# Optimization experiments

Hardware: AMD Instinct MI355X
Metric: run time of the kernel (lower is better)

## Reference

```python
import jax, jax.numpy as jnp
import numpy as np

NUM_USERS = 100000
NUM_ITEMS = 100000
N_NODES = NUM_USERS + NUM_ITEMS
EMB = 64
N_EDGES = 3200000
N_LAYERS = 3


def setup_inputs() -> dict:
    key = jax.random.key(0)
    k1, k2, k3, k4, k5 = jax.random.split(key, 5)
    user_emb = jax.random.normal(k1, (NUM_USERS, EMB), dtype=jnp.float32)
    item_emb = jax.random.normal(k2, (NUM_ITEMS, EMB), dtype=jnp.float32)
    # COO representation of the normalized adjacency norm_adj (values ~ 1/sqrt(d_i d_j))
    edge_row = jax.random.randint(k3, (N_EDGES,), 0, N_NODES, dtype=jnp.int32)
    edge_col = jax.random.randint(k4, (N_EDGES,), 0, N_NODES, dtype=jnp.int32)
    edge_w = jax.random.uniform(k5, (N_EDGES,), dtype=jnp.float32)
    return {"user_emb": user_emb, "item_emb": item_emb, "edge_w": edge_w,
            "edge_row": edge_row, "edge_col": edge_col}


def _spmm(edge_row, edge_col, edge_w, x):
    # y[r] = sum_{e: row[e]==r} w[e] * x[col[e]]  ==  torch.sparse.mm(norm_adj, x)
    msgs = edge_w[:, None] * x[edge_col]  # [n_edges, E]
    return jax.ops.segment_sum(msgs, edge_row, num_segments=N_NODES)


def reference(user_emb, item_emb, edge_w, edge_row, edge_col):
    ego = jnp.concatenate([user_emb, item_emb], axis=0)  # [N, E]
    acc = jnp.zeros_like(ego)
    for _ in range(N_LAYERS):
        ego = _spmm(edge_row, edge_col, edge_w, ego)
        acc = acc + ego
    final = acc / N_LAYERS  # mean over the n_layers propagated embeddings
    user_all = final[:NUM_USERS]
    item_all = final[NUM_USERS:]
    return (user_all, item_all)
```

## Files before the change

### kernel.cpp

```cpp
#include <hip/hip_runtime.h>
#include <hip/hip_bf16.h>


constexpr int NUM_USERS = 100000;
constexpr int NUM_ITEMS = 100000;
constexpr int N_NODES   = NUM_USERS + NUM_ITEMS;
constexpr int EMB       = 64;
constexpr int N_EDGES   = 3200000;

constexpr int BUCK_SHIFT = 8;
constexpr int NBUCK = (N_NODES + 255) >> BUCK_SHIFT;
constexpr int BIN_BLOCK = 512;
constexpr int EPB = 8192;
constexpr int NBIN_BLOCKS = (N_EDGES + EPB - 1) / EPB;
constexpr int SORT_CAP = 6144;

constexpr int HIST_BLOCKS   = 512;
constexpr int CONCAT_BLOCKS = (N_NODES * 8 + 255) / 256;

constexpr int ROWS_PER_BLOCK = 32;
constexpr int ECAP = 1536;


__device__ __forceinline__ float bfl(unsigned u) { return __uint_as_float(u << 16); }
__device__ __forceinline__ float bfh(unsigned u) { return __uint_as_float(u & 0xFFFF0000u); }
__device__ __forceinline__ unsigned f2bf(float f) {
    unsigned u = __float_as_uint(f);
    return (u + 0x7FFFu + ((u >> 16) & 1u)) >> 16;
}
__device__ __forceinline__ unsigned pk(float lo, float hi) {
    return f2bf(lo) | (f2bf(hi) << 16);
}


__global__ __launch_bounds__(256) void prep(
    const int* __restrict__ row, int* __restrict__ bcnt,
    const float4* __restrict__ u, const float4* __restrict__ it,
    uint4* __restrict__ ebuf) {
    __shared__ int h[NBUCK];
    if (blockIdx.x < HIST_BLOCKS) {
        for (int i = threadIdx.x; i < NBUCK; i += 256) h[i] = 0;
        __syncthreads();
        int nt = HIST_BLOCKS * 256;
        for (int e = blockIdx.x * 256 + threadIdx.x; e < N_EDGES; e += nt) {
            int r = __builtin_nontemporal_load(&row[e]);
            atomicAdd(&h[r >> BUCK_SHIFT], 1);
        }
        __syncthreads();
        for (int i = threadIdx.x; i < NBUCK; i += 256) {
            int c = h[i];
            if (c) atomicAdd(&bcnt[i], c);
        }
    } else {
        int i = (blockIdx.x - HIST_BLOCKS) * 256 + threadIdx.x;
        if (i >= N_NODES * 8) return;
        const float4* s = (i < NUM_USERS * 8) ? (u + 2 * (size_t)i)
                                              : (it + 2 * ((size_t)i - (size_t)NUM_USERS * 8));
        float4 f0 = s[0], f1 = s[1];
        uint4 o;
        o.x = pk(f0.x, f0.y); o.y = pk(f0.z, f0.w);
        o.z = pk(f1.x, f1.y); o.w = pk(f1.z, f1.w);
        ebuf[i] = o;
    }
}


__global__ __launch_bounds__(1024) void scan_buckets(const int* __restrict__ bcnt,
                                                     int* __restrict__ bbase,
                                                     int* __restrict__ bcursor) {
    __shared__ int lds[1024];
    int t = threadIdx.x;
    int v = (t < NBUCK) ? bcnt[t] : 0;
    lds[t] = v;
    __syncthreads();
    for (int off = 1; off < 1024; off <<= 1) {
        int x = (t >= off) ? lds[t - off] : 0;
        __syncthreads();
        lds[t] += x;
        __syncthreads();
    }
    int excl = lds[t] - v;
    if (t < NBUCK) { bbase[t] = excl; bcursor[t] = excl; }
    if (t == 0) bbase[NBUCK] = N_EDGES;
}

__global__ __launch_bounds__(BIN_BLOCK) void bin_edges(
    const int* __restrict__ row, const int* __restrict__ col,
    const float* __restrict__ w,
    int* __restrict__ bcursor, int2* __restrict__ binned) {
    __shared__ int2 stage[EPB];
    __shared__ int  hcnt[NBUCK];
    __shared__ int  hbase[NBUCK];
    __shared__ int  cursor[NBUCK];
    __shared__ int  lds2[BIN_BLOCK];
    int t = threadIdx.x;
    int e0 = blockIdx.x * EPB;
    int e1 = e0 + EPB; if (e1 > N_EDGES) e1 = N_EDGES;

    for (int i = t; i < NBUCK; i += BIN_BLOCK) hcnt[i] = 0;
    __syncthreads();
    for (int e = e0 + t; e < e1; e += BIN_BLOCK)
        atomicAdd(&hcnt[row[e] >> BUCK_SHIFT], 1);
    __syncthreads();

    for (int i = t; i < NBUCK; i += BIN_BLOCK) {
        int c = hcnt[i];
        hbase[i] = c ? atomicAdd(&bcursor[i], c) : 0;
    }
    int i0 = 2 * t, i1 = 2 * t + 1;
    int c0 = (i0 < NBUCK) ? hcnt[i0] : 0;
    int c1 = (i1 < NBUCK) ? hcnt[i1] : 0;
    lds2[t] = c0 + c1;
    __syncthreads();
    for (int off = 1; off < BIN_BLOCK; off <<= 1) {
        int x = (t >= off) ? lds2[t - off] : 0;
        __syncthreads();
        lds2[t] += x;
        __syncthreads();
    }
    int pairExcl = lds2[t] - (c0 + c1);
    if (i0 < NBUCK) cursor[i0] = pairExcl;
    if (i1 < NBUCK) cursor[i1] = pairExcl + c0;
    __syncthreads();

    for (int e = e0 + t; e < e1; e += BIN_BLOCK) {
        int r  = row[e];
        int bk = r >> BUCK_SHIFT;
        int pos = atomicAdd(&cursor[bk], 1);
        stage[pos] = make_int2(__builtin_nontemporal_load(&col[e]) | ((r & 255) << 18),
                               __float_as_int(__builtin_nontemporal_load(&w[e])));
    }
    __syncthreads();

    int wave = t >> 6;
    int lane = t & 63;
    int sl   = lane & 7;
    constexpr int NWAVE = BIN_BLOCK / 64;
    for (int base = wave * 8; base < NBUCK; base += NWAVE * 8) {
        int bk = base + (lane >> 3);
        if (bk < NBUCK) {
            int c  = hcnt[bk];
            int st = cursor[bk] - c;
            int gp = hbase[bk];
            for (int j = sl; j < c; j += 8)
                binned[gp + j] = stage[st + j];
        }
    }
}

__global__ __launch_bounds__(256) void sort_bucket(
    const int* __restrict__ bbase, const int2* __restrict__ binned,
    int2* __restrict__ sorted, int* __restrict__ row_start) {
    __shared__ int cnt[256];
    __shared__ int sc[256];
    __shared__ int2 buf[SORT_CAP];
    int b = blockIdx.x, t = threadIdx.x;
    int gb = bbase[b];
    int n  = bbase[b + 1] - gb;

    cnt[t] = 0;
    __syncthreads();
    for (int i = t; i < n; i += 256)
        atomicAdd(&cnt[binned[gb + i].x >> 18], 1);
    __syncthreads();

    int v = cnt[t];
    sc[t] = v;
    __syncthreads();
    for (int off = 1; off < 256; off <<= 1) {
        int x = (t >= off) ? sc[t - off] : 0;
        __syncthreads();
        sc[t] += x;
        __syncthreads();
    }
    int excl = sc[t] - v;

    int r = (b << BUCK_SHIFT) + t;
    if (r < N_NODES) row_start[r] = gb + excl;
    if (b == NBUCK - 1 && t == 0) row_start[N_NODES] = N_EDGES;
    __syncthreads();
    cnt[t] = excl;
    __syncthreads();

    for (int i = t; i < n; i += 256) {
        int2 rec = binned[gb + i];
        int rl = rec.x >> 18;
        int k = atomicAdd(&cnt[rl], 1);
        if (k < SORT_CAP)
            buf[k] = make_int2(rec.x & 0x3FFFF, rec.y);
    }
    __syncthreads();
    int m = n < SORT_CAP ? n : SORT_CAP;
    for (int i = t; i < m; i += 256)
        sorted[gb + i] = buf[i];
}


template<bool LAST>
__global__ __launch_bounds__(256) void spmm_bf16(
    const int* __restrict__ row_start, const int2* __restrict__ sorted,
    const uint4* __restrict__ src,
    uint4* __restrict__ y,
    const uint4* __restrict__ y1,
    float4* __restrict__ out)
{
    __shared__ int2 erec[ECAP];
    __shared__ int  rs[ROWS_PER_BLOCK + 1];
    int t  = threadIdx.x;
    int R0 = blockIdx.x * ROWS_PER_BLOCK;
    if (t <= ROWS_PER_BLOCK) rs[t] = row_start[R0 + t];
    __syncthreads();
    int eb0 = rs[0];
    int n   = rs[ROWS_PER_BLOCK] - eb0;

    int g = t >> 3;
    int s = t & 7;
    int r = R0 + g;
    int s0 = rs[g], s1 = rs[g + 1];
    int cnt = s1 - s0;

    float a0 = 0.f, a1 = 0.f, a2 = 0.f, a3 = 0.f;
    float a4 = 0.f, a5 = 0.f, a6 = 0.f, a7 = 0.f;

#define ACC(vv, wt) \
    a0 = fmaf(wt, bfl(vv.x), a0); a1 = fmaf(wt, bfh(vv.x), a1); \
    a2 = fmaf(wt, bfl(vv.y), a2); a3 = fmaf(wt, bfh(vv.y), a3); \
    a4 = fmaf(wt, bfl(vv.z), a4); a5 = fmaf(wt, bfh(vv.z), a5); \
    a6 = fmaf(wt, bfl(vv.w), a6); a7 = fmaf(wt, bfh(vv.w), a7);

    if (n <= ECAP) {
        for (int i = t; i < n; i += 256) erec[i] = sorted[eb0 + i];
        __syncthreads();
        int lb = s0 - eb0;
        for (int k = 0; k < cnt; k += 8) {
            int   c[8]; float wv[8]; uint4 gr[8];
#pragma unroll
            for (int j = 0; j < 8; ++j) {
                int lk = k + j;
                bool v = lk < cnt;
                int2 e = erec[lb + (v ? lk : 0)];
                c[j]  = v ? e.x : 0;
                wv[j] = v ? __int_as_float(e.y) : 0.f;
            }
#pragma unroll
            for (int j = 0; j < 8; ++j) gr[j] = src[(size_t)c[j] * 8 + s];
#pragma unroll
            for (int j = 0; j < 8; ++j) { ACC(gr[j], wv[j]) }
        }
    } else {
        for (int k = 0; k < cnt; k += 8) {
            int   c[8]; float wv[8]; uint4 gr[8];
#pragma unroll
            for (int j = 0; j < 8; ++j) {
                int lk = k + j;
                bool v = lk < cnt;
                int2 e = sorted[s0 + (v ? lk : 0)];
                c[j]  = v ? e.x : 0;
                wv[j] = v ? __int_as_float(e.y) : 0.f;
            }
#pragma unroll
            for (int j = 0; j < 8; ++j) gr[j] = src[(size_t)c[j] * 8 + s];
#pragma unroll
            for (int j = 0; j < 8; ++j) { ACC(gr[j], wv[j]) }
        }
    }
#undef ACC

    if (!LAST) {
        uint4 o;
        o.x = pk(a0, a1); o.y = pk(a2, a3);
        o.z = pk(a4, a5); o.w = pk(a6, a7);
        y[(size_t)r * 8 + s] = o;
    } else {
        uint4 u1 = y1[(size_t)r * 8 + s];
        uint4 u2 = src[(size_t)r * 8 + s];
        constexpr float sc = 1.0f / 3.0f;
        float4 o0, o1;
        o0.x = (a0 + bfl(u1.x) + bfl(u2.x)) * sc;
        o0.y = (a1 + bfh(u1.x) + bfh(u2.x)) * sc;
        o0.z = (a2 + bfl(u1.y) + bfl(u2.y)) * sc;
        o0.w = (a3 + bfh(u1.y) + bfh(u2.y)) * sc;
        o1.x = (a4 + bfl(u1.z) + bfl(u2.z)) * sc;
        o1.y = (a5 + bfh(u1.z) + bfh(u2.z)) * sc;
        o1.z = (a6 + bfl(u1.w) + bfl(u2.w)) * sc;
        o1.w = (a7 + bfh(u1.w) + bfh(u2.w)) * sc;
        size_t ob = (size_t)r * 16 + 2 * s;
        out[ob]     = o0;
        out[ob + 1] = o1;
    }
}


extern "C" void kernel_launch(void* const* d_in, const int* in_sizes, int n_in,
                              void* d_out, int out_size, void* d_ws, size_t ws_size,
                              hipStream_t stream) {
    const float* user_emb = (const float*)d_in[0];
    const float* item_emb = (const float*)d_in[1];
    const float* edge_w   = (const float*)d_in[2];
    const int*   edge_row = (const int*)d_in[3];
    const int*   edge_col = (const int*)d_in[4];

    char* p = (char*)d_ws;
    uint4* ebuf = (uint4*)p;        p += (size_t)N_NODES * 8 * sizeof(uint4);
    uint4* ybuf = (uint4*)p;        p += (size_t)N_NODES * 8 * sizeof(uint4);
    int2*  sorted = (int2*)p;       p += (size_t)N_EDGES * sizeof(int2);
    int*   bcnt = (int*)p;          p += (size_t)NBUCK * sizeof(int);
    int*   bbase = (int*)p;         p += (size_t)(NBUCK + 1) * sizeof(int);
    int*   bcursor = (int*)p;       p += (size_t)NBUCK * sizeof(int);
    int*   row_start = (int*)p;     p += (size_t)(N_NODES + 1) * sizeof(int);
    int2*  binned = (int2*)ybuf;

    hipMemsetAsync(bcnt, 0, (size_t)NBUCK * sizeof(int), stream);

    prep<<<HIST_BLOCKS + CONCAT_BLOCKS, 256, 0, stream>>>(
        edge_row, bcnt, (const float4*)user_emb, (const float4*)item_emb, ebuf);

    scan_buckets<<<1, 1024, 0, stream>>>(bcnt, bbase, bcursor);
    bin_edges<<<NBIN_BLOCKS, BIN_BLOCK, 0, stream>>>(edge_row, edge_col, edge_w,
                                                     bcursor, binned);
    sort_bucket<<<NBUCK, 256, 0, stream>>>(bbase, binned, sorted, row_start);

    int grid = N_NODES / ROWS_PER_BLOCK;
    spmm_bf16<false><<<grid, 256, 0, stream>>>(row_start, sorted, ebuf, ybuf,
                                               nullptr, nullptr);
    spmm_bf16<false><<<grid, 256, 0, stream>>>(row_start, sorted, ybuf, ebuf,
                                               nullptr, nullptr);
    spmm_bf16<true><<<grid, 256, 0, stream>>>(row_start, sorted, ebuf, nullptr,
                                              ybuf, (float4*)d_out);
}
```

Measured before the change: 404.3 us.

## Split embedding into two column halves and pack edges into 32-bit records

Stores the bf16 embedding as two 32-column halves and runs the three propagation layers separately per half, so each pass gathers from a 6.4MB table that is more likely to stay cache-resident. Edge records shrink from 8 to 4 bytes by packing an 18-bit column index with a 14-bit quantized weight. The sort kernel now stages records in LDS before counting. The cost is twice as many SpMM launches and re-reading the edge list twice. The 14-bit fixed-point weight adds quantization error and relies on weights lying in [0,1).

New measurement: 497.3 us. +23.0%, slower.

```diff
diff --git a/kernel.cpp b/kernel.cpp
--- a/kernel.cpp
+++ b/kernel.cpp
@@ -18,8 +18,8 @@
 constexpr int HIST_BLOCKS   = 512;
 constexpr int CONCAT_BLOCKS = (N_NODES * 8 + 255) / 256;
 
-constexpr int ROWS_PER_BLOCK = 32;
-constexpr int ECAP = 1536;
+constexpr int SROWS = 64;
+constexpr int ECAP  = 2560;
 
 
 __device__ __forceinline__ float bfl(unsigned u) { return __uint_as_float(u << 16); }
@@ -52,15 +52,20 @@
             if (c) atomicAdd(&bcnt[i], c);
         }
     } else {
-        int i = (blockIdx.x - HIST_BLOCKS) * 256 + threadIdx.x;
-        if (i >= N_NODES * 8) return;
-        const float4* s = (i < NUM_USERS * 8) ? (u + 2 * (size_t)i)
-                                              : (it + 2 * ((size_t)i - (size_t)NUM_USERS * 8));
-        float4 f0 = s[0], f1 = s[1];
+        int j = (blockIdx.x - HIST_BLOCKS) * 256 + threadIdx.x;
+        if (j >= N_NODES * 8) return;
+        int hf   = (j >= N_NODES * 4) ? 1 : 0;
+        int idx  = j - hf * N_NODES * 4;
+        int node = idx >> 2;
+        int s    = idx & 3;
+        const float4* sp = (node < NUM_USERS)
+            ? (u  + (size_t)node * 16 + hf * 8 + s * 2)
+            : (it + (size_t)(node - NUM_USERS) * 16 + hf * 8 + s * 2);
+        float4 f0 = sp[0], f1 = sp[1];
         uint4 o;
         o.x = pk(f0.x, f0.y); o.y = pk(f0.z, f0.w);
         o.z = pk(f1.x, f1.y); o.w = pk(f1.z, f1.w);
-        ebuf[i] = o;
+        ebuf[j] = o;
     }
 }
 
@@ -150,18 +155,21 @@
 
 __global__ __launch_bounds__(256) void sort_bucket(
     const int* __restrict__ bbase, const int2* __restrict__ binned,
-    int2* __restrict__ sorted, int* __restrict__ row_start) {
+    unsigned* __restrict__ sorted, int* __restrict__ row_start) {
+    __shared__ int2     raw[SORT_CAP];
+    __shared__ unsigned buf[SORT_CAP];
     __shared__ int cnt[256];
     __shared__ int sc[256];
-    __shared__ int2 buf[SORT_CAP];
     int b = blockIdx.x, t = threadIdx.x;
     int gb = bbase[b];
     int n  = bbase[b + 1] - gb;
+    int m  = n < SORT_CAP ? n : SORT_CAP;
 
     cnt[t] = 0;
-    __syncthreads();
-    for (int i = t; i < n; i += 256)
-        atomicAdd(&cnt[binned[gb + i].x >> 18], 1);
+    for (int i = t; i < m; i += 256) raw[i] = binned[gb + i];
+    __syncthreads();
+    for (int i = t; i < m; i += 256)
+        atomicAdd(&cnt[raw[i].x >> 18], 1);
     __syncthreads();
 
     int v = cnt[t];
@@ -182,45 +190,48 @@
     cnt[t] = excl;
     __syncthreads();
 
-    for (int i = t; i < n; i += 256) {
-        int2 rec = binned[gb + i];
+    for (int i = t; i < m; i += 256) {
+        int2 rec = raw[i];
         int rl = rec.x >> 18;
         int k = atomicAdd(&cnt[rl], 1);
-        if (k < SORT_CAP)
-            buf[k] = make_int2(rec.x & 0x3FFFF, rec.y);
-    }
-    __syncthreads();
-    int m = n < SORT_CAP ? n : SORT_CAP;
+        float wv = __int_as_float(rec.y);
+        unsigned q = (unsigned)(wv * 16384.f + 0.5f);
+        if (q > 16383u) q = 16383u;
+        buf[k] = ((unsigned)rec.x & 0x3FFFFu) | (q << 18);
+    }
+    __syncthreads();
     for (int i = t; i < m; i += 256)
         sorted[gb + i] = buf[i];
 }
 
 
 template<bool LAST>
-__global__ __launch_bounds__(256) void spmm_bf16(
-    const int* __restrict__ row_start, const int2* __restrict__ sorted,
+__global__ __launch_bounds__(256) void spmm_half(
+    const int* __restrict__ row_start, const unsigned* __restrict__ sorted,
     const uint4* __restrict__ src,
     uint4* __restrict__ y,
     const uint4* __restrict__ y1,
-    float4* __restrict__ out)
+    float4* __restrict__ out,
+    int half)
 {
-    __shared__ int2 erec[ECAP];
-    __shared__ int  rs[ROWS_PER_BLOCK + 1];
+    __shared__ unsigned erec[ECAP];
+    __shared__ int rs[SROWS + 1];
     int t  = threadIdx.x;
-    int R0 = blockIdx.x * ROWS_PER_BLOCK;
-    if (t <= ROWS_PER_BLOCK) rs[t] = row_start[R0 + t];
+    int R0 = blockIdx.x * SROWS;
+    if (t <= SROWS) rs[t] = row_start[R0 + t];
     __syncthreads();
     int eb0 = rs[0];
-    int n   = rs[ROWS_PER_BLOCK] - eb0;
-
-    int g = t >> 3;
-    int s = t & 7;
+    int n   = rs[SROWS] - eb0;
+
+    int g = t >> 2;
+    int s = t & 3;
     int r = R0 + g;
     int s0 = rs[g], s1 = rs[g + 1];
     int cnt = s1 - s0;
 
     float a0 = 0.f, a1 = 0.f, a2 = 0.f, a3 = 0.f;
     float a4 = 0.f, a5 = 0.f, a6 = 0.f, a7 = 0.f;
+    constexpr float WSC = 1.0f / 16384.f;
 
 #define ACC(vv, wt) \
     a0 = fmaf(wt, bfl(vv.x), a0); a1 = fmaf(wt, bfh(vv.x), a1); \
@@ -238,12 +249,12 @@
             for (int j = 0; j < 8; ++j) {
                 int lk = k + j;
                 bool v = lk < cnt;
-                int2 e = erec[lb + (v ? lk : 0)];
-                c[j]  = v ? e.x : 0;
-                wv[j] = v ? __int_as_float(e.y) : 0.f;
+                unsigned e = erec[lb + (v ? lk : 0)];
+                c[j]  = v ? (int)(e & 0x3FFFFu) : 0;
+                wv[j] = v ? (float)(e >> 18) * WSC : 0.f;
             }
 #pragma unroll
-            for (int j = 0; j < 8; ++j) gr[j] = src[(size_t)c[j] * 8 + s];
+            for (int j = 0; j < 8; ++j) gr[j] = src[(size_t)c[j] * 4 + s];
 #pragma unroll
             for (int j = 0; j < 8; ++j) { ACC(gr[j], wv[j]) }
         }
@@ -254,12 +265,12 @@
             for (int j = 0; j < 8; ++j) {
                 int lk = k + j;
                 bool v = lk < cnt;
-                int2 e = sorted[s0 + (v ? lk : 0)];
-                c[j]  = v ? e.x : 0;
-                wv[j] = v ? __int_as_float(e.y) : 0.f;
+                unsigned e = sorted[s0 + (v ? lk : 0)];
+                c[j]  = v ? (int)(e & 0x3FFFFu) : 0;
+                wv[j] = v ? (float)(e >> 18) * WSC : 0.f;
             }
 #pragma unroll
-            for (int j = 0; j < 8; ++j) gr[j] = src[(size_t)c[j] * 8 + s];
+            for (int j = 0; j < 8; ++j) gr[j] = src[(size_t)c[j] * 4 + s];
 #pragma unroll
             for (int j = 0; j < 8; ++j) { ACC(gr[j], wv[j]) }
         }
@@ -270,10 +281,10 @@
         uint4 o;
         o.x = pk(a0, a1); o.y = pk(a2, a3);
         o.z = pk(a4, a5); o.w = pk(a6, a7);
-        y[(size_t)r * 8 + s] = o;
+        y[(size_t)r * 4 + s] = o;
     } else {
-        uint4 u1 = y1[(size_t)r * 8 + s];
-        uint4 u2 = src[(size_t)r * 8 + s];
+        uint4 u1 = y1[(size_t)r * 4 + s];
+        uint4 u2 = src[(size_t)r * 4 + s];
         constexpr float sc = 1.0f / 3.0f;
         float4 o0, o1;
         o0.x = (a0 + bfl(u1.x) + bfl(u2.x)) * sc;
@@ -284,7 +295,7 @@
         o1.y = (a5 + bfh(u1.z) + bfh(u2.z)) * sc;
         o1.z = (a6 + bfl(u1.w) + bfl(u2.w)) * sc;
         o1.w = (a7 + bfh(u1.w) + bfh(u2.w)) * sc;
-        size_t ob = (size_t)r * 16 + 2 * s;
+        size_t ob = (size_t)r * 16 + half * 8 + s * 2;
         out[ob]     = o0;
         out[ob + 1] = o1;
     }
@@ -301,9 +312,9 @@
     const int*   edge_col = (const int*)d_in[4];
 
     char* p = (char*)d_ws;
-    uint4* ebuf = (uint4*)p;        p += (size_t)N_NODES * 8 * sizeof(uint4);
-    uint4* ybuf = (uint4*)p;        p += (size_t)N_NODES * 8 * sizeof(uint4);
-    int2*  sorted = (int2*)p;       p += (size_t)N_EDGES * sizeof(int2);
+    uint4*    ebuf = (uint4*)p;     p += (size_t)N_NODES * 8 * sizeof(uint4);
+    uint4*    ybuf = (uint4*)p;     p += (size_t)N_NODES * 8 * sizeof(uint4);
+    unsigned* sorted = (unsigned*)p; p += (size_t)N_EDGES * sizeof(unsigned);
     int*   bcnt = (int*)p;          p += (size_t)NBUCK * sizeof(int);
     int*   bbase = (int*)p;         p += (size_t)(NBUCK + 1) * sizeof(int);
     int*   bcursor = (int*)p;       p += (size_t)NBUCK * sizeof(int);
@@ -320,11 +331,17 @@
                                                      bcursor, binned);
     sort_bucket<<<NBUCK, 256, 0, stream>>>(bbase, binned, sorted, row_start);
 
-    int grid = N_NODES / ROWS_PER_BLOCK;
-    spmm_bf16<false><<<grid, 256, 0, stream>>>(row_start, sorted, ebuf, ybuf,
-                                               nullptr, nullptr);
-    spmm_bf16<false><<<grid, 256, 0, stream>>>(row_start, sorted, ybuf, ebuf,
-                                               nullptr, nullptr);
-    spmm_bf16<true><<<grid, 256, 0, stream>>>(row_start, sorted, ebuf, nullptr,
-                                              ybuf, (float4*)d_out);
-}
+    uint4* e0 = ebuf;
+    uint4* e1 = ebuf + (size_t)N_NODES * 4;
+    uint4* y0 = ybuf;
+    uint4* y1p = ybuf + (size_t)N_NODES * 4;
+    float4* out = (float4*)d_out;
+    int grid = N_NODES / SROWS;
+
+    spmm_half<false><<<grid, 256, 0, stream>>>(row_start, sorted, e0, y0, nullptr, nullptr, 0);
+    spmm_half<false><<<grid, 256, 0, stream>>>(row_start, sorted, y0, e0, nullptr, nullptr, 0);
+    spmm_half<true ><<<grid, 256, 0, stream>>>(row_start, sorted, e0, nullptr, y0, out, 0);
+    spmm_half<false><<<grid, 256, 0, stream>>>(row_start, sorted, e1, y1p, nullptr, nullptr, 1);
+    spmm_half<false><<<grid, 256, 0, stream>>>(row_start, sorted, y1p, e1, nullptr, nullptr, 1);
+    spmm_half<true ><<<grid, 256, 0, stream>>>(row_start, sorted, e1, nullptr, y1p, out, 1);
+}
```

## Pack edge column and 14-bit quantized weight into one 32-bit record

Applied to the files above, without the earlier changes.

Edge weights are quantized to 14-bit fixed point and packed with the 18-bit column index into a single 32-bit word, halving the sorted edge array read by each SpMM layer. The row-local index moves to a separate byte array during binning, and the sort kernel now stages raw records in shared memory. This cuts memory traffic in binning, sorting and the three propagation passes, at the cost of weight precision and the assumption that weights lie in [0,1].

Measured after the change: 392.9 us. 1.03x faster.

```diff
diff --git a/kernel.cpp b/kernel.cpp
--- a/kernel.cpp
+++ b/kernel.cpp
@@ -87,8 +87,10 @@
 __global__ __launch_bounds__(BIN_BLOCK) void bin_edges(
     const int* __restrict__ row, const int* __restrict__ col,
     const float* __restrict__ w,
-    int* __restrict__ bcursor, int2* __restrict__ binned) {
-    __shared__ int2 stage[EPB];
+    int* __restrict__ bcursor,
+    unsigned* __restrict__ binned_cw, unsigned char* __restrict__ binned_rl) {
+    __shared__ unsigned      stage_cw[EPB];
+    __shared__ unsigned char stage_rl[EPB];
     __shared__ int  hcnt[NBUCK];
     __shared__ int  hbase[NBUCK];
     __shared__ int  cursor[NBUCK];
@@ -127,8 +129,11 @@
         int r  = row[e];
         int bk = r >> BUCK_SHIFT;
         int pos = atomicAdd(&cursor[bk], 1);
-        stage[pos] = make_int2(__builtin_nontemporal_load(&col[e]) | ((r & 255) << 18),
-                               __float_as_int(__builtin_nontemporal_load(&w[e])));
+        float wv = __builtin_nontemporal_load(&w[e]);
+        unsigned q = (unsigned)(wv * 16384.f + 0.5f);
+        if (q > 16383u) q = 16383u;
+        stage_cw[pos] = (unsigned)__builtin_nontemporal_load(&col[e]) | (q << 18);
+        stage_rl[pos] = (unsigned char)(r & 255);
     }
     __syncthreads();
 
@@ -142,26 +147,36 @@
             int c  = hcnt[bk];
             int st = cursor[bk] - c;
             int gp = hbase[bk];
-            for (int j = sl; j < c; j += 8)
-                binned[gp + j] = stage[st + j];
+            for (int j = sl; j < c; j += 8) {
+                binned_cw[gp + j] = stage_cw[st + j];
+                binned_rl[gp + j] = stage_rl[st + j];
+            }
         }
     }
 }
 
 __global__ __launch_bounds__(256) void sort_bucket(
-    const int* __restrict__ bbase, const int2* __restrict__ binned,
-    int2* __restrict__ sorted, int* __restrict__ row_start) {
+    const int* __restrict__ bbase,
+    const unsigned* __restrict__ binned_cw, const unsigned char* __restrict__ binned_rl,
+    unsigned* __restrict__ sorted, int* __restrict__ row_start) {
+    __shared__ unsigned      raw_cw[SORT_CAP];
+    __shared__ unsigned char raw_rl[SORT_CAP];
+    __shared__ unsigned      buf[SORT_CAP];
     __shared__ int cnt[256];
     __shared__ int sc[256];
-    __shared__ int2 buf[SORT_CAP];
     int b = blockIdx.x, t = threadIdx.x;
     int gb = bbase[b];
     int n  = bbase[b + 1] - gb;
+    int m  = n < SORT_CAP ? n : SORT_CAP;
 
     cnt[t] = 0;
-    __syncthreads();
-    for (int i = t; i < n; i += 256)
-        atomicAdd(&cnt[binned[gb + i].x >> 18], 1);
+    for (int i = t; i < m; i += 256) {
+        raw_cw[i] = binned_cw[gb + i];
+        raw_rl[i] = binned_rl[gb + i];
+    }
+    __syncthreads();
+    for (int i = t; i < m; i += 256)
+        atomicAdd(&cnt[raw_rl[i]], 1);
     __syncthreads();
 
     int v = cnt[t];
@@ -182,15 +197,11 @@
     cnt[t] = excl;
     __syncthreads();
 
-    for (int i = t; i < n; i += 256) {
-        int2 rec = binned[gb + i];
-        int rl = rec.x >> 18;
-        int k = atomicAdd(&cnt[rl], 1);
-        if (k < SORT_CAP)
-            buf[k] = make_int2(rec.x & 0x3FFFF, rec.y);
-    }
-    __syncthreads();
-    int m = n < SORT_CAP ? n : SORT_CAP;
+    for (int i = t; i < m; i += 256) {
+        int k = atomicAdd(&cnt[raw_rl[i]], 1);
+        buf[k] = raw_cw[i];
+    }
+    __syncthreads();
     for (int i = t; i < m; i += 256)
         sorted[gb + i] = buf[i];
 }
@@ -198,14 +209,14 @@
 
 template<bool LAST>
 __global__ __launch_bounds__(256) void spmm_bf16(
-    const int* __restrict__ row_start, const int2* __restrict__ sorted,
+    const int* __restrict__ row_start, const unsigned* __restrict__ sorted,
     const uint4* __restrict__ src,
     uint4* __restrict__ y,
     const uint4* __restrict__ y1,
     float4* __restrict__ out)
 {
-    __shared__ int2 erec[ECAP];
-    __shared__ int  rs[ROWS_PER_BLOCK + 1];
+    __shared__ unsigned erec[ECAP];
+    __shared__ int rs[ROWS_PER_BLOCK + 1];
     int t  = threadIdx.x;
     int R0 = blockIdx.x * ROWS_PER_BLOCK;
     if (t <= ROWS_PER_BLOCK) rs[t] = row_start[R0 + t];
@@ -221,6 +232,7 @@
 
     float a0 = 0.f, a1 = 0.f, a2 = 0.f, a3 = 0.f;
     float a4 = 0.f, a5 = 0.f, a6 = 0.f, a7 = 0.f;
+    constexpr float WSC = 1.0f / 16384.f;
 
 #define ACC(vv, wt) \
     a0 = fmaf(wt, bfl(vv.x), a0); a1 = fmaf(wt, bfh(vv.x), a1); \
@@ -238,9 +250,9 @@
             for (int j = 0; j < 8; ++j) {
                 int lk = k + j;
                 bool v = lk < cnt;
-                int2 e = erec[lb + (v ? lk : 0)];
-                c[j]  = v ? e.x : 0;
-                wv[j] = v ? __int_as_float(e.y) : 0.f;
+                unsigned e = erec[lb + (v ? lk : 0)];
+                c[j]  = v ? (int)(e & 0x3FFFFu) : 0;
+                wv[j] = v ? (float)(e >> 18) * WSC : 0.f;
             }
 #pragma unroll
             for (int j = 0; j < 8; ++j) gr[j] = src[(size_t)c[j] * 8 + s];
@@ -254,9 +266,9 @@
             for (int j = 0; j < 8; ++j) {
                 int lk = k + j;
                 bool v = lk < cnt;
-                int2 e = sorted[s0 + (v ? lk : 0)];
-                c[j]  = v ? e.x : 0;
-                wv[j] = v ? __int_as_float(e.y) : 0.f;
+                unsigned e = sorted[s0 + (v ? lk : 0)];
+                c[j]  = v ? (int)(e & 0x3FFFFu) : 0;
+                wv[j] = v ? (float)(e >> 18) * WSC : 0.f;
             }
 #pragma unroll
             for (int j = 0; j < 8; ++j) gr[j] = src[(size_t)c[j] * 8 + s];
@@ -301,14 +313,15 @@
     const int*   edge_col = (const int*)d_in[4];
 
     char* p = (char*)d_ws;
-    uint4* ebuf = (uint4*)p;        p += (size_t)N_NODES * 8 * sizeof(uint4);
-    uint4* ybuf = (uint4*)p;        p += (size_t)N_NODES * 8 * sizeof(uint4);
-    int2*  sorted = (int2*)p;       p += (size_t)N_EDGES * sizeof(int2);
-    int*   bcnt = (int*)p;          p += (size_t)NBUCK * sizeof(int);
-    int*   bbase = (int*)p;         p += (size_t)(NBUCK + 1) * sizeof(int);
-    int*   bcursor = (int*)p;       p += (size_t)NBUCK * sizeof(int);
-    int*   row_start = (int*)p;     p += (size_t)(N_NODES + 1) * sizeof(int);
-    int2*  binned = (int2*)ybuf;
+    uint4*    ebuf = (uint4*)p;      p += (size_t)N_NODES * 8 * sizeof(uint4);
+    uint4*    ybuf = (uint4*)p;      p += (size_t)N_NODES * 8 * sizeof(uint4);
+    unsigned* sorted = (unsigned*)p; p += (size_t)N_EDGES * sizeof(unsigned);
+    int*   bcnt = (int*)p;           p += (size_t)NBUCK * sizeof(int);
+    int*   bbase = (int*)p;          p += (size_t)(NBUCK + 1) * sizeof(int);
+    int*   bcursor = (int*)p;        p += (size_t)NBUCK * sizeof(int);
+    int*   row_start = (int*)p;      p += (size_t)(N_NODES + 1) * sizeof(int);
+    unsigned*      binned_cw = (unsigned*)ybuf;
+    unsigned char* binned_rl = (unsigned char*)(ybuf) + (size_t)N_EDGES * 4;
 
     hipMemsetAsync(bcnt, 0, (size_t)NBUCK * sizeof(int), stream);
 
@@ -317,8 +330,9 @@
 
     scan_buckets<<<1, 1024, 0, stream>>>(bcnt, bbase, bcursor);
     bin_edges<<<NBIN_BLOCKS, BIN_BLOCK, 0, stream>>>(edge_row, edge_col, edge_w,
-                                                     bcursor, binned);
-    sort_bucket<<<NBUCK, 256, 0, stream>>>(bbase, binned, sorted, row_start);
+                                                     bcursor, binned_cw, binned_rl);
+    sort_bucket<<<NBUCK, 256, 0, stream>>>(bbase, binned_cw, binned_rl,
+                                           sorted, row_start);
 
     int grid = N_NODES / ROWS_PER_BLOCK;
     spmm_bf16<false><<<grid, 256, 0, stream>>>(row_start, sorted, ebuf, ybuf,
```
